# Kernel tuning notes

Hardware: AMD Instinct MI355X
Metric: run time of the kernel (lower is better)

The kernel has to match this reference:

```python
import jax, jax.numpy as jnp
import numpy as np


def setup_inputs() -> dict:
    key = jax.random.key(0)
    k1, k2, k3, k4 = jax.random.split(key, 4)
    B, C = 32768, 10
    x = jax.random.normal(k1, (B, 1, 28, 28), dtype=jnp.float32)
    linear_weight = jax.random.normal(k2, (4 * 14 * 14 + 1 + 2, C), dtype=jnp.float32)
    linear_bias = jax.random.normal(k3, (C,), dtype=jnp.float32)
    sampler_weights = jax.random.normal(k4, (4,), dtype=jnp.float32)
    return {"x": x, "linear_weight": linear_weight, "linear_bias": linear_bias,
            "sampler_weights": sampler_weights}


def reference(x, linear_weight, linear_bias, sampler_weights):
    # Closed-form simulation of the 4-qubit circuits:
    # RY(t)|0> -> <Z>=cos(t); after CX(0,1): <Z1> = cos(t0)*cos(t1); CX(2,3) likewise.
    B = x.shape[0]
    # Extract non-overlapping 2x2 patches in row-major order -> (B, 196, 4)
    p = x[:, 0].reshape(B, 14, 2, 14, 2).transpose(0, 1, 3, 2, 4).reshape(B, 196, 4)
    c = jnp.cos(p)
    # quanvolution_circuit per patch: [cos a, cos a cos b, cos c, cos c cos d]
    feats = jnp.stack([c[..., 0], c[..., 0] * c[..., 1],
                       c[..., 2], c[..., 2] * c[..., 3]], axis=-1)  # (B,196,4)
    qfeat = feats.reshape(B, 784)
    # fully_connected_circuit on qfeat[:, :4]: mean of the four post-CX <Z>
    cf = jnp.cos(qfeat[:, :4])
    qfc = (cf[:, 0] + cf[:, 0] * cf[:, 1] + cf[:, 2] + cf[:, 2] * cf[:, 3]) / 4.0  # (B,)
    # sampler_circuit: sequential RY angles add on wires 0 and 1
    t0 = qfeat[:, 0] + sampler_weights[0] + sampler_weights[2]
    t1 = qfeat[:, 1] + sampler_weights[1] + sampler_weights[3]
    z0 = jnp.cos(t0)
    z1 = z0 * jnp.cos(t1)
    sampler = jax.nn.softmax(jnp.stack([z0, z1], axis=-1), axis=-1)  # (B,2)
    combined = jnp.concatenate([qfeat, qfc[:, None], sampler], axis=-1)  # (B,787)
    logits = combined @ linear_weight + linear_bias
    return jax.nn.log_softmax(logits, axis=-1)
```

## Files before the change

### kernel.cpp

```cpp
#include <hip/hip_runtime.h>


typedef __attribute__((ext_vector_type(8))) short short8;
typedef __attribute__((ext_vector_type(4))) float floatx4;

__device__ __forceinline__ unsigned short f2bf(float f) {
    unsigned u = __float_as_uint(f);
    return (unsigned short)((u + 0x7FFFu + ((u >> 16) & 1u)) >> 16);
}

#define SCR_OFF 28672
#define QF_OFF  60160

__global__ __launch_bounds__(256, 2)
void qml_mfma(const float* __restrict__ x,
              const float* __restrict__ wm,
              const float* __restrict__ bias,
              const float* __restrict__ sw,
              float* __restrict__ out,
              int B)
{
    __shared__ __align__(16) char smem[61184];
    float* rawW = (float*)(smem + SCR_OFF);
    float* lg   = (float*)(smem + SCR_OFF);
    float* qf   = (float*)(smem + QF_OFF);

    const int t = threadIdx.x;
    const int lane = t & 63;
    const int wv = __builtin_amdgcn_readfirstlane((int)(t >> 6));
    const int g = blockIdx.x;

    for (int i = t; i < 7870; i += 256) rawW[i] = wm[i];
    __syncthreads();

#pragma unroll
    for (int c = 0; c < 7; ++c) {
        const int CH = c * 256 + t;
        const int T = CH >> 6, L = CH & 63;
        const int n = L & 15, kq = L >> 4;
        short8 v;
#pragma unroll
        for (int j = 0; j < 8; ++j) {
            const int kh = 32 * T + kq * 8 + j;
            const int sg = kh >> 7, kl = kh & 127;
            float w = 0.0f;
            if (kl < 112 && n < 10) w = rawW[(112 * sg + kl) * 10 + n];
            v[j] = (short)f2bf(w);
        }
        *(short8*)(smem + CH * 16) = v;
    }
    __syncthreads();

    const int m = lane & 15;
    const int q = lane >> 4;
    int sample = g * 64 + wv * 16 + m;
    const bool s_ok = (sample < B);
    if (sample >= B) sample = B - 1;
    const float* __restrict__ xs = x + (size_t)sample * 784;

    int offT[4], validT[4];
#pragma unroll
    for (int T = 0; T < 4; ++T) {
        const int pr = 4 * T + q;
        validT[T] = (pr < 14);
        const int r = (pr >= 7) ? 1 : 0;
        const int cq = (pr >= 7) ? (pr - 7) : pr;
        offT[T] = validT[T] ? (r * 56 + 4 * cq) : 0;
    }

    floatx4 tp[3][4], bt[3][4];

#define LOADSTRIP(slot, sg_)                                            \
    {                                                                   \
        _Pragma("unroll")                                               \
        for (int T = 0; T < 4; ++T) {                                   \
            tp[slot][T] = *(const floatx4*)(xs + (sg_) * 112 + offT[T]);        \
            bt[slot][T] = *(const floatx4*)(xs + (sg_) * 112 + offT[T] + 28);   \
        }                                                               \
    }

    floatx4 acc = {0.f, 0.f, 0.f, 0.f};

    LOADSTRIP(0, 0)
    LOADSTRIP(1, 1)

#pragma unroll
    for (int sg = 0; sg < 7; ++sg) {
        const int slot = sg % 3;
        if (sg < 5) {
            const int ns = (sg + 2) % 3;
            LOADSTRIP(ns, sg + 2)
        }

#pragma unroll
        for (int T = 0; T < 4; ++T) {
            const floatx4 P = tp[slot][T];
            const floatx4 Q = bt[slot][T];
            const float c0 = __cosf(P.x), c1 = __cosf(P.y);
            const float c2 = __cosf(Q.x), c3 = __cosf(Q.y);
            const float c4 = __cosf(P.z), c5 = __cosf(P.w);
            const float c6 = __cosf(Q.z), c7 = __cosf(Q.w);
            const float f0 = c0, f1 = c0 * c1, f2 = c2, f3 = c2 * c3;
            const float f4 = c4, f5 = c4 * c5, f6 = c6, f7 = c6 * c7;

            if (sg == 0 && T == 0 && q == 0) {
                float* qd = qf + (wv * 16 + m) * 4;
                qd[0] = f0; qd[1] = f1; qd[2] = f2; qd[3] = f3;
            }

            short8 a;
            a[0] = (short)f2bf(f0); a[1] = (short)f2bf(f1);
            a[2] = (short)f2bf(f2); a[3] = (short)f2bf(f3);
            a[4] = (short)f2bf(f4); a[5] = (short)f2bf(f5);
            a[6] = (short)f2bf(f6); a[7] = (short)f2bf(f7);
            if (!validT[T]) {
                a = (short8){0, 0, 0, 0, 0, 0, 0, 0};
            }

            const short8 b8 = *(const short8*)(smem + ((4 * sg + T) * 64 + lane) * 16);
            acc = __builtin_amdgcn_mfma_f32_16x16x32_bf16(a, b8, acc, 0, 0, 0);
        }
    }

    {
        const int n = lane & 15;
        const int rbase = wv * 16 + (lane >> 4) * 4;
        if (n < 10) {
#pragma unroll
            for (int r = 0; r < 4; ++r) lg[(rbase + r) * 11 + n] = acc[r];
        }
    }
    __syncthreads();

#pragma unroll
    for (int e = t; e < 640; e += 256) {
        const int s2 = e / 10, c2 = e - 10 * s2;
        float logit = lg[s2 * 11 + c2];
        const float q0 = qf[s2 * 4 + 0], q1 = qf[s2 * 4 + 1];
        const float q2 = qf[s2 * 4 + 2], q3 = qf[s2 * 4 + 3];

        const float f0 = __cosf(q0), f1 = __cosf(q1);
        const float f2 = __cosf(q2), f3 = __cosf(q3);
        const float qfc = (f0 + f0 * f1 + f2 + f2 * f3) * 0.25f;

        const float t0 = q0 + sw[0] + sw[2];
        const float t1 = q1 + sw[1] + sw[3];
        const float z0 = __cosf(t0);
        const float z1 = z0 * __cosf(t1);
        const float e0 = __expf(z0), e1 = __expf(z1);
        const float inv = 1.0f / (e0 + e1);

        const float* __restrict__ wt = wm + 7840;
        logit += bias[c2] + qfc * wt[c2] + (e0 * inv) * wt[10 + c2]
                          + (e1 * inv) * wt[20 + c2];
        lg[s2 * 11 + c2] = logit;
    }
    __syncthreads();

#pragma unroll
    for (int e = t; e < 640; e += 256) {
        const int s2 = e / 10, c2 = e - 10 * s2;
        float mx = -3.4e38f;
#pragma unroll
        for (int k = 0; k < 10; ++k) mx = fmaxf(mx, lg[s2 * 11 + k]);
        float ss = 0.0f;
#pragma unroll
        for (int k = 0; k < 10; ++k) ss += __expf(lg[s2 * 11 + k] - mx);
        const float lse = __logf(ss) + mx;
        if (g * 64 + s2 < B)
            out[(size_t)g * 640 + e] = lg[s2 * 11 + c2] - lse;
    }
}

extern "C" void kernel_launch(void* const* d_in, const int* in_sizes, int n_in,
                              void* d_out, int out_size, void* d_ws, size_t ws_size,
                              hipStream_t stream) {
    const float* x    = (const float*)d_in[0];
    const float* w    = (const float*)d_in[1];
    const float* bias = (const float*)d_in[2];
    const float* sw   = (const float*)d_in[3];
    float* out = (float*)d_out;

    const int B = in_sizes[0] / 784;
    const int nblk = (B + 63) / 64;
    qml_mfma<<<nblk, 256, 0, stream>>>(x, w, bias, sw, out, B);
}
```

Baseline: 161.3 us.

## Stage input strips through per-wave LDS with coalesced global loads

Each wave now loads its 16 samples' 112-float strips with lane-contiguous 16-byte global reads into registers. It then writes them into a per-wave padded LDS staging area, and the MFMA loop reads its patch operands from there. Before, each lane fetched scattered 16-byte pieces at a per-sample stride. The first two strips are issued before the weight-repack phase, so their latency overlaps that setup, and a triple-buffered register ring keeps the prefetch two strips ahead. The cost is extra LDS traffic and space, plus reliance on in-order LDS access within a wave, since no barrier guards the staging buffer.

```diff
diff --git a/kernel.cpp b/kernel.cpp
--- a/kernel.cpp
+++ b/kernel.cpp
@@ -9,8 +9,11 @@
     return (unsigned short)((u + 0x7FFFu + ((u >> 16) & 1u)) >> 16);
 }
 
-#define SCR_OFF 28672
-#define QF_OFF  60160
+#define STG_OFF 28672
+#define STG_WV  7424
+#define QF_OFF  58368
+#define LG_OFF  59392
+#define SMEM_SZ 62208
 
 __global__ __launch_bounds__(256, 2)
 void qml_mfma(const float* __restrict__ x,
@@ -20,15 +23,34 @@
               float* __restrict__ out,
               int B)
 {
-    __shared__ __align__(16) char smem[61184];
-    float* rawW = (float*)(smem + SCR_OFF);
-    float* lg   = (float*)(smem + SCR_OFF);
+    __shared__ __align__(16) char smem[SMEM_SZ];
+    float* rawW = (float*)(smem + STG_OFF);
     float* qf   = (float*)(smem + QF_OFF);
+    float* lg   = (float*)(smem + LG_OFF);
 
     const int t = threadIdx.x;
     const int lane = t & 63;
     const int wv = __builtin_amdgcn_readfirstlane((int)(t >> 6));
     const int g = blockIdx.x;
+
+    const float* gp[7];
+    int lofs[7];
+#pragma unroll
+    for (int i = 0; i < 7; ++i) {
+        const int c = i * 64 + lane;
+        const int s = (c * 37450) >> 20;
+        const int off = c - 28 * s;
+        int sgl = g * 64 + wv * 16 + s;
+        if (sgl >= B) sgl = B - 1;
+        gp[i] = x + (size_t)sgl * 784 + off * 4;
+        lofs[i] = STG_OFF + wv * STG_WV + s * 464 + off * 16;
+    }
+
+    floatx4 rr[3][7];
+#pragma unroll
+    for (int i = 0; i < 7; ++i) rr[0][i] = *(const floatx4*)(gp[i]);
+#pragma unroll
+    for (int i = 0; i < 7; ++i) rr[1][i] = *(const floatx4*)(gp[i] + 112);
 
     for (int i = t; i < 7870; i += 256) rawW[i] = wm[i];
     __syncthreads();
@@ -51,51 +73,30 @@
     }
     __syncthreads();
 
+#pragma unroll
+    for (int i = 0; i < 7; ++i) *(floatx4*)(smem + lofs[i]) = rr[0][i];
+
     const int m = lane & 15;
     const int q = lane >> 4;
-    int sample = g * 64 + wv * 16 + m;
-    const bool s_ok = (sample < B);
-    if (sample >= B) sample = B - 1;
-    const float* __restrict__ xs = x + (size_t)sample * 784;
-
-    int offT[4], validT[4];
+    int offB[4], validT[4];
 #pragma unroll
     for (int T = 0; T < 4; ++T) {
         const int pr = 4 * T + q;
         validT[T] = (pr < 14);
         const int r = (pr >= 7) ? 1 : 0;
         const int cq = (pr >= 7) ? (pr - 7) : pr;
-        offT[T] = validT[T] ? (r * 56 + 4 * cq) : 0;
+        offB[T] = validT[T] ? (r * 224 + cq * 16) : 0;
     }
-
-    floatx4 tp[3][4], bt[3][4];
-
-#define LOADSTRIP(slot, sg_)                                            \
-    {                                                                   \
-        _Pragma("unroll")                                               \
-        for (int T = 0; T < 4; ++T) {                                   \
-            tp[slot][T] = *(const floatx4*)(xs + (sg_) * 112 + offT[T]);        \
-            bt[slot][T] = *(const floatx4*)(xs + (sg_) * 112 + offT[T] + 28);   \
-        }                                                               \
-    }
+    const char* myrow = smem + STG_OFF + wv * STG_WV + m * 464;
 
     floatx4 acc = {0.f, 0.f, 0.f, 0.f};
 
-    LOADSTRIP(0, 0)
-    LOADSTRIP(1, 1)
-
 #pragma unroll
     for (int sg = 0; sg < 7; ++sg) {
-        const int slot = sg % 3;
-        if (sg < 5) {
-            const int ns = (sg + 2) % 3;
-            LOADSTRIP(ns, sg + 2)
-        }
-
 #pragma unroll
         for (int T = 0; T < 4; ++T) {
-            const floatx4 P = tp[slot][T];
-            const floatx4 Q = bt[slot][T];
+            const floatx4 P = *(const floatx4*)(myrow + offB[T]);
+            const floatx4 Q = *(const floatx4*)(myrow + offB[T] + 112);
             const float c0 = __cosf(P.x), c1 = __cosf(P.y);
             const float c2 = __cosf(Q.x), c3 = __cosf(Q.y);
             const float c4 = __cosf(P.z), c5 = __cosf(P.w);
@@ -113,12 +114,21 @@
             a[2] = (short)f2bf(f2); a[3] = (short)f2bf(f3);
             a[4] = (short)f2bf(f4); a[5] = (short)f2bf(f5);
             a[6] = (short)f2bf(f6); a[7] = (short)f2bf(f7);
-            if (!validT[T]) {
-                a = (short8){0, 0, 0, 0, 0, 0, 0, 0};
-            }
+            if (!validT[T]) a = (short8){0, 0, 0, 0, 0, 0, 0, 0};
 
             const short8 b8 = *(const short8*)(smem + ((4 * sg + T) * 64 + lane) * 16);
             acc = __builtin_amdgcn_mfma_f32_16x16x32_bf16(a, b8, acc, 0, 0, 0);
+        }
+        if (sg < 6) {
+            const int ws = (sg + 1) % 3;
+#pragma unroll
+            for (int i = 0; i < 7; ++i) *(floatx4*)(smem + lofs[i]) = rr[ws][i];
+            if (sg < 5) {
+                const int ns = (sg + 2) % 3;
+#pragma unroll
+                for (int i = 0; i < 7; ++i)
+                    rr[ns][i] = *(const floatx4*)(gp[i] + (sg + 2) * 112);
+            }
         }
     }
 
```

Result: no change. 161.9 us (+0.4%).
